# Performance work log

Hardware: AMD Instinct MI355X
Metric: run time of the kernel (lower is better)

## Reference

```python
import jax, jax.numpy as jnp
import numpy as np

LN_EPS = 1e-5

def _layer_norm(x, gamma, beta):
    mu = jnp.mean(x, axis=-1, keepdims=True)
    var = jnp.mean(jnp.square(x - mu), axis=-1, keepdims=True)
    return (x - mu) * jax.lax.rsqrt(var + LN_EPS) * gamma + beta

def setup_inputs() -> dict:
    key = jax.random.key(0)
    ks = jax.random.split(key, 6)
    B, Lc, S, H = 8, 16384, 2048, 256
    char_embeddings = jax.random.normal(ks[0], (B, Lc, H), dtype=jnp.float32)
    # include some negative indices (-1, -2) to exercise the no-token mask path
    token_alignment = jax.random.randint(ks[1], (B, Lc), -2, S, dtype=jnp.int32).astype(jnp.int64)
    decoder_hidden_states = jax.random.normal(ks[2], (B, S, H), dtype=jnp.float32)
    scale1 = 1.0 / np.sqrt(2 * H)
    W1 = jax.random.normal(ks[3], (2 * H, H), dtype=jnp.float32) * scale1
    b1 = jnp.zeros((H,), dtype=jnp.float32)
    W2 = jax.random.normal(ks[4], (2 * H, H), dtype=jnp.float32) * scale1
    b2 = jnp.zeros((H,), dtype=jnp.float32)
    ln_gamma = jnp.ones((H,), dtype=jnp.float32)
    ln_beta = jnp.zeros((H,), dtype=jnp.float32)
    return {
        "char_embeddings": char_embeddings,
        "token_alignment": token_alignment,
        "decoder_hidden_states": decoder_hidden_states,
        "W1": W1, "b1": b1, "W2": W2, "b2": b2,
        "ln_gamma": ln_gamma, "ln_beta": ln_beta,
    }

def reference(char_embeddings, token_alignment, decoder_hidden_states,
              W1, b1, W2, b2, ln_gamma, ln_beta):
    B, Lc, H = char_embeddings.shape
    S = decoder_hidden_states.shape[1]
    # per-character gather of decoder token representations (vectorized over batch)
    valid_idx = jnp.clip(token_alignment, 0, S - 1)                         # [B, Lc]
    tok_reprs = jnp.take_along_axis(decoder_hidden_states,
                                    valid_idx[..., None].astype(jnp.int32),
                                    axis=1)                                  # [B, Lc, H]
    tok_reprs = jnp.where((token_alignment < 0)[..., None], 0.0, tok_reprs)
    # alignment_network: Linear(2H -> H)
    combined = jnp.concatenate([char_embeddings, tok_reprs], axis=-1)        # [B, Lc, 2H]
    aligned = jnp.einsum('blk,kh->blh', combined, W1) + b1                   # [B, Lc, H]
    # syllable_feature_extractor: Linear(2H->H) + LayerNorm + GELU (+ eval-mode Dropout)
    combined2 = jnp.concatenate([char_embeddings, aligned], axis=-1)         # [B, Lc, 2H]
    feats = jnp.einsum('blk,kh->blh', combined2, W2) + b2
    feats = _layer_norm(feats, ln_gamma, ln_beta)
    feats = jax.nn.gelu(feats, approximate=False)                            # torch nn.GELU exact
    return char_embeddings + feats
```

## Files before the change

### kernel.cpp

```cpp
#include <hip/hip_runtime.h>
#include <hip/hip_bf16.h>
#include <math.h>
#include <stdint.h>

#define H     256
#define K2    512
#define SDEC  2048
#define LCSH  14
#define BM    64
#define BK    64
#define NTHR  256

typedef __attribute__((ext_vector_type(8))) short  short8;
typedef __attribute__((ext_vector_type(4))) float  f32x4;

typedef __attribute__((address_space(3))) unsigned int lds_u32;
typedef __attribute__((address_space(1))) unsigned int glb_u32;

__device__ __forceinline__ void async_ld16(const void* g, void* l) {
  __builtin_amdgcn_global_load_lds((const glb_u32*)(uintptr_t)g,
                                   (lds_u32*)(uintptr_t)l, 16, 0, 0);
}

__device__ __forceinline__ unsigned short f2bf(float f) {
  union { float f; unsigned int u; } c; c.f = f;
  unsigned int u = c.u;
  unsigned int r = u + 0x7fffu + ((u >> 16) & 1u);
  return (unsigned short)(r >> 16);
}

__global__ __launch_bounds__(256) void fuse_weights(
    const float* __restrict__ W1, const float* __restrict__ W2,
    unsigned short* __restrict__ wft) {
  __shared__ float As[64][65];
  __shared__ float Bs[64][65];
  const int t  = threadIdx.x;
  const int k0 = (blockIdx.x >> 2) * 64;
  const int n0 = (blockIdx.x & 3) * 64;
  const int lr = t >> 2;
  const int ls = t & 3;
  const int tk = t >> 4;
  const int tn = t & 15;

  float acc[4][4];
#pragma unroll
  for (int i = 0; i < 4; ++i)
#pragma unroll
    for (int c = 0; c < 4; ++c) acc[i][c] = 0.0f;

  for (int jt = 0; jt < 4; ++jt) {
    const int j0 = jt * 64;
    __syncthreads();
    const float* a_src = W1 + (size_t)(k0 + lr) * H + j0 + ls * 16;
    const float* b_src = W2 + (size_t)(H + j0 + lr) * H + n0 + ls * 16;
#pragma unroll
    for (int i = 0; i < 16; ++i) {
      As[lr][ls * 16 + i] = a_src[i];
      Bs[lr][ls * 16 + i] = b_src[i];
    }
    __syncthreads();
#pragma unroll 8
    for (int j = 0; j < 64; ++j) {
      float a[4], b[4];
#pragma unroll
      for (int i = 0; i < 4; ++i) a[i] = As[tk * 4 + i][j];
#pragma unroll
      for (int c = 0; c < 4; ++c) b[c] = Bs[j][tn * 4 + c];
#pragma unroll
      for (int i = 0; i < 4; ++i)
#pragma unroll
        for (int c = 0; c < 4; ++c) acc[i][c] += a[i] * b[c];
    }
  }

#pragma unroll
  for (int i = 0; i < 4; ++i) {
    const int k = k0 + tk * 4 + i;
#pragma unroll
    for (int c = 0; c < 4; ++c) {
      const int n = n0 + tn * 4 + c;
      float v = acc[i][c];
      if (k < H) v += W2[(size_t)k * H + n];
      wft[(size_t)n * K2 + k] = f2bf(v);
    }
  }
}

__global__ __launch_bounds__(256) void fuse_bias(
    const float* __restrict__ W2, const float* __restrict__ b1,
    const float* __restrict__ b2, float* __restrict__ biasf) {
  const int n = threadIdx.x;
  float acc = b2[n];
  for (int j = 0; j < H; ++j) acc += b1[j] * W2[(size_t)(H + j) * H + n];
  biasf[n] = acc;
}

__global__ __launch_bounds__(NTHR, 2) void syl_main(
    const float* __restrict__ cemb, const int* __restrict__ tal,
    const float* __restrict__ dec, const unsigned short* __restrict__ wft,
    const float* __restrict__ biasf, const float* __restrict__ gamma,
    const float* __restrict__ beta, float* __restrict__ out) {

  __shared__ __align__(16) unsigned short Ash[BM][72];
  __shared__ __align__(16) unsigned short Bsh[H][BK];
  __shared__ int   idxs[BM];
  __shared__ float msks[BM];
  __shared__ float stats[4][BM][2];

  const int t    = threadIdx.x;
  const int wave = t >> 6;
  const int lane = t & 63;
  const int quad = lane >> 4;
  const int l15  = lane & 15;
  const int row0 = blockIdx.x * BM;
  const int bidx = row0 >> LCSH;
  const float* decb = dec + (size_t)bidx * SDEC * H;

  if (t < BM) {
    int ix = tal[row0 + t];
    idxs[t] = ix < 0 ? 0 : (ix >= SDEC ? SDEC - 1 : ix);
    msks[t] = ix < 0 ? 0.0f : 1.0f;
  }

  f32x4 acc[4][4];
#pragma unroll
  for (int m = 0; m < 4; ++m)
#pragma unroll
    for (int n = 0; n < 4; ++n) acc[m][n] = (f32x4){0.f, 0.f, 0.f, 0.f};

  const int srow = t >> 2;
  const int sseg = t & 3;

  for (int ki = 0; ki < 8; ++ki) {
    const int k0 = ki * BK;

#pragma unroll
    for (int c = 0; c < 8; ++c) {
      const int nrow = wave * 64 + c * 8;
      const unsigned short* g =
          wft + (size_t)(nrow + (lane >> 3)) * K2 + k0 + (lane & 7) * 8;
      async_ld16(g, &Bsh[nrow][0]);
    }

    const float* src;
    float scale;
    if (k0 < H) {
      src = cemb + (size_t)(row0 + srow) * H + k0 + sseg * 16;
      scale = 1.0f;
    } else {
      src = decb + (size_t)idxs[srow] * H + (k0 - H) + sseg * 16;
      scale = msks[srow];
    }
    float4 f[4];
#pragma unroll
    for (int q = 0; q < 4; ++q) f[q] = *(const float4*)(src + q * 4);
    unsigned short hb[16];
#pragma unroll
    for (int q = 0; q < 4; ++q) {
      hb[q * 4 + 0] = f2bf(f[q].x * scale);
      hb[q * 4 + 1] = f2bf(f[q].y * scale);
      hb[q * 4 + 2] = f2bf(f[q].z * scale);
      hb[q * 4 + 3] = f2bf(f[q].w * scale);
    }
    *(short8*)&Ash[srow][sseg * 16]     = *(short8*)&hb[0];
    *(short8*)&Ash[srow][sseg * 16 + 8] = *(short8*)&hb[8];

    __syncthreads();

    short8 af[2][4];
#pragma unroll
    for (int ks = 0; ks < 2; ++ks)
#pragma unroll
      for (int m = 0; m < 4; ++m)
        af[ks][m] = *(const short8*)&Ash[m * 16 + l15][ks * 32 + quad * 8];
#pragma unroll
    for (int ks = 0; ks < 2; ++ks)
#pragma unroll
      for (int n = 0; n < 4; ++n) {
        short8 bf = *(const short8*)&Bsh[wave * 64 + n * 16 + l15][ks * 32 + quad * 8];
#pragma unroll
        for (int m = 0; m < 4; ++m)
          acc[m][n] = __builtin_amdgcn_mfma_f32_16x16x32_bf16(
              af[ks][m], bf, acc[m][n], 0, 0, 0);
      }
    __syncthreads();
  }

  float bvals[4], gvals[4], betv[4];
#pragma unroll
  for (int n = 0; n < 4; ++n) {
    const int col = wave * 64 + n * 16 + l15;
    bvals[n] = biasf[col];
    gvals[n] = gamma[col];
    betv[n]  = beta[col];
  }
#pragma unroll
  for (int m = 0; m < 4; ++m)
#pragma unroll
    for (int n = 0; n < 4; ++n)
#pragma unroll
      for (int r = 0; r < 4; ++r) acc[m][n][r] += bvals[n];

#pragma unroll
  for (int m = 0; m < 4; ++m)
#pragma unroll
    for (int r = 0; r < 4; ++r) {
      float a = 0.f, b = 0.f;
#pragma unroll
      for (int n = 0; n < 4; ++n) {
        const float v = acc[m][n][r];
        a += v; b += v * v;
      }
#pragma unroll
      for (int d = 1; d < 16; d <<= 1) {
        a += __shfl_xor(a, d, 64);
        b += __shfl_xor(b, d, 64);
      }
      if (l15 == 0) {
        const int row = m * 16 + quad * 4 + r;
        stats[wave][row][0] = a;
        stats[wave][row][1] = b;
      }
    }
  __syncthreads();

  float mean_[4][4], rstd_[4][4];
#pragma unroll
  for (int m = 0; m < 4; ++m)
#pragma unroll
    for (int r = 0; r < 4; ++r) {
      const int row = m * 16 + quad * 4 + r;
      const float a = stats[0][row][0] + stats[1][row][0] +
                      stats[2][row][0] + stats[3][row][0];
      const float b = stats[0][row][1] + stats[1][row][1] +
                      stats[2][row][1] + stats[3][row][1];
      const float mu  = a * (1.0f / 256.0f);
      const float var = b * (1.0f / 256.0f) - mu * mu;
      mean_[m][r] = mu;
      rstd_[m][r] = rsqrtf(var + 1e-5f);
    }

#pragma unroll
  for (int m = 0; m < 4; ++m) {
#pragma unroll
    for (int r = 0; r < 4; ++r) {
      const size_t row = (size_t)row0 + m * 16 + quad * 4 + r;
      const float* crow = cemb + row * H;
      float* orow = out + row * H;
#pragma unroll
      for (int n = 0; n < 4; ++n) {
        const int col = wave * 64 + n * 16 + l15;
        const float x = (acc[m][n][r] - mean_[m][r]) * rstd_[m][r];
        const float y = x * gvals[n] + betv[n];
        const float g = 0.5f * y * (1.0f + erff(y * 0.70710678118654752f));
        orow[col] = crow[col] + g;
      }
    }
  }
}

extern "C" void kernel_launch(void* const* d_in, const int* in_sizes, int n_in,
                              void* d_out, int out_size, void* d_ws, size_t ws_size,
                              hipStream_t stream) {
  const float* cemb  = (const float*)d_in[0];
  const int*   tal   = (const int*)d_in[1];
  const float* dec   = (const float*)d_in[2];
  const float* W1    = (const float*)d_in[3];
  const float* b1    = (const float*)d_in[4];
  const float* W2    = (const float*)d_in[5];
  const float* b2    = (const float*)d_in[6];
  const float* gamma = (const float*)d_in[7];
  const float* beta  = (const float*)d_in[8];
  float* out = (float*)d_out;

  unsigned short* wft = (unsigned short*)d_ws;
  float* biasf = (float*)((char*)d_ws + (size_t)K2 * H * sizeof(unsigned short));

  const int rows = in_sizes[0] / H;

  hipLaunchKernelGGL(fuse_weights, dim3(32), dim3(256), 0, stream, W1, W2, wft);
  hipLaunchKernelGGL(fuse_bias, dim3(1), dim3(256), 0, stream, W2, b1, b2, biasf);
  hipLaunchKernelGGL(syl_main, dim3(rows / BM), dim3(NTHR), 0, stream,
                     cemb, tal, dec, wft, biasf, gamma, beta, out);
}
```

Baseline: 405.8 us.

## Load B fragments from global into registers, double-buffer A, stage epilogue through LDS

The main GEMM kernel stops staging the fused weight tile in LDS. Each wave now reads its bf16 B fragments straight from global memory (L2-resident) into registers. The A tile is double-buffered in a fragment-ordered LDS layout, so the next K-slice's global loads overlap the current MFMAs, leaving one barrier per iteration. The epilogue writes GELU results into LDS and then emits coalesced float4 residual reads and output stores instead of scattered scalar accesses. Occupancy is raised to 3 blocks per SM through the smaller LDS footprint, at the cost of redundant per-wave weight loads from cache and extra barriers in the epilogue.

```diff
diff --git a/kernel.cpp b/kernel.cpp
--- a/kernel.cpp
+++ b/kernel.cpp
@@ -13,14 +13,6 @@
 
 typedef __attribute__((ext_vector_type(8))) short  short8;
 typedef __attribute__((ext_vector_type(4))) float  f32x4;
-
-typedef __attribute__((address_space(3))) unsigned int lds_u32;
-typedef __attribute__((address_space(1))) unsigned int glb_u32;
-
-__device__ __forceinline__ void async_ld16(const void* g, void* l) {
-  __builtin_amdgcn_global_load_lds((const glb_u32*)(uintptr_t)g,
-                                   (lds_u32*)(uintptr_t)l, 16, 0, 0);
-}
 
 __device__ __forceinline__ unsigned short f2bf(float f) {
   union { float f; unsigned int u; } c; c.f = f;
@@ -95,14 +87,16 @@
   biasf[n] = acc;
 }
 
-__global__ __launch_bounds__(NTHR, 2) void syl_main(
+__global__ __launch_bounds__(NTHR, 3) void syl_main(
     const float* __restrict__ cemb, const int* __restrict__ tal,
     const float* __restrict__ dec, const unsigned short* __restrict__ wft,
     const float* __restrict__ biasf, const float* __restrict__ gamma,
     const float* __restrict__ beta, float* __restrict__ out) {
 
-  __shared__ __align__(16) unsigned short Ash[BM][72];
-  __shared__ __align__(16) unsigned short Bsh[H][BK];
+  __shared__ __align__(16) char smem[16640];
+  unsigned short* AshC = (unsigned short*)smem;
+  float* Ef = (float*)smem;
+
   __shared__ int   idxs[BM];
   __shared__ float msks[BM];
   __shared__ float stats[4][BM][2];
@@ -130,60 +124,85 @@
 
   const int srow = t >> 2;
   const int sseg = t & 3;
-
+  const int ksS  = sseg >> 1;
+  const int qS   = (sseg & 1) * 2;
+  const int mS   = srow >> 4;
+  const int l15S = srow & 15;
+  const int wchunk0 = (ksS * 4 + mS) * 64 + qS * 16 + l15S;
+
+  {
+    const float* src = cemb + (size_t)(row0 + srow) * H + sseg * 16;
+    float4 f[4];
+#pragma unroll
+    for (int q = 0; q < 4; ++q) f[q] = *(const float4*)(src + q * 4);
+    unsigned short hb[16];
+#pragma unroll
+    for (int q = 0; q < 4; ++q) {
+      hb[q * 4 + 0] = f2bf(f[q].x); hb[q * 4 + 1] = f2bf(f[q].y);
+      hb[q * 4 + 2] = f2bf(f[q].z); hb[q * 4 + 3] = f2bf(f[q].w);
+    }
+    *(short8*)(AshC + (size_t)wchunk0 * 8)        = *(short8*)&hb[0];
+    *(short8*)(AshC + (size_t)(wchunk0 + 16) * 8) = *(short8*)&hb[8];
+  }
+  __syncthreads();
+
+  int buf = 0;
   for (int ki = 0; ki < 8; ++ki) {
     const int k0 = ki * BK;
 
-#pragma unroll
-    for (int c = 0; c < 8; ++c) {
-      const int nrow = wave * 64 + c * 8;
-      const unsigned short* g =
-          wft + (size_t)(nrow + (lane >> 3)) * K2 + k0 + (lane & 7) * 8;
-      async_ld16(g, &Bsh[nrow][0]);
-    }
-
-    const float* src;
-    float scale;
-    if (k0 < H) {
-      src = cemb + (size_t)(row0 + srow) * H + k0 + sseg * 16;
-      scale = 1.0f;
-    } else {
-      src = decb + (size_t)idxs[srow] * H + (k0 - H) + sseg * 16;
-      scale = msks[srow];
-    }
+    short8 bf[2][4];
+#pragma unroll
+    for (int ks = 0; ks < 2; ++ks)
+#pragma unroll
+      for (int n = 0; n < 4; ++n) {
+        const unsigned short* bp =
+            wft + (size_t)(wave * 64 + n * 16 + l15) * K2 + k0 + ks * 32 + quad * 8;
+        bf[ks][n] = *(const short8*)bp;
+      }
+
     float4 f[4];
-#pragma unroll
-    for (int q = 0; q < 4; ++q) f[q] = *(const float4*)(src + q * 4);
-    unsigned short hb[16];
-#pragma unroll
-    for (int q = 0; q < 4; ++q) {
-      hb[q * 4 + 0] = f2bf(f[q].x * scale);
-      hb[q * 4 + 1] = f2bf(f[q].y * scale);
-      hb[q * 4 + 2] = f2bf(f[q].z * scale);
-      hb[q * 4 + 3] = f2bf(f[q].w * scale);
-    }
-    *(short8*)&Ash[srow][sseg * 16]     = *(short8*)&hb[0];
-    *(short8*)&Ash[srow][sseg * 16 + 8] = *(short8*)&hb[8];
-
-    __syncthreads();
-
-    short8 af[2][4];
-#pragma unroll
-    for (int ks = 0; ks < 2; ++ks)
+    float scale = 1.0f;
+    if (ki < 7) {
+      const int k0n = k0 + BK;
+      const float* src;
+      if (k0n < H) {
+        src = cemb + (size_t)(row0 + srow) * H + k0n + sseg * 16;
+      } else {
+        src = decb + (size_t)idxs[srow] * H + (k0n - H) + sseg * 16;
+        scale = msks[srow];
+      }
+#pragma unroll
+      for (int q = 0; q < 4; ++q) f[q] = *(const float4*)(src + q * 4);
+    }
+
+#pragma unroll
+    for (int ks = 0; ks < 2; ++ks) {
+      short8 af[4];
 #pragma unroll
       for (int m = 0; m < 4; ++m)
-        af[ks][m] = *(const short8*)&Ash[m * 16 + l15][ks * 32 + quad * 8];
-#pragma unroll
-    for (int ks = 0; ks < 2; ++ks)
-#pragma unroll
-      for (int n = 0; n < 4; ++n) {
-        short8 bf = *(const short8*)&Bsh[wave * 64 + n * 16 + l15][ks * 32 + quad * 8];
+        af[m] = *(const short8*)(AshC +
+                 (size_t)(((buf * 2 + ks) * 4 + m) * 64 + lane) * 8);
+#pragma unroll
+      for (int n = 0; n < 4; ++n)
 #pragma unroll
         for (int m = 0; m < 4; ++m)
           acc[m][n] = __builtin_amdgcn_mfma_f32_16x16x32_bf16(
-              af[ks][m], bf, acc[m][n], 0, 0, 0);
-      }
-    __syncthreads();
+              af[m], bf[ks][n], acc[m][n], 0, 0, 0);
+    }
+
+    if (ki < 7) {
+      unsigned short hb[16];
+#pragma unroll
+      for (int q = 0; q < 4; ++q) {
+        hb[q * 4 + 0] = f2bf(f[q].x * scale); hb[q * 4 + 1] = f2bf(f[q].y * scale);
+        hb[q * 4 + 2] = f2bf(f[q].z * scale); hb[q * 4 + 3] = f2bf(f[q].w * scale);
+      }
+      const int nb = buf ^ 1;
+      *(short8*)(AshC + (size_t)(nb * 512 + wchunk0) * 8)      = *(short8*)&hb[0];
+      *(short8*)(AshC + (size_t)(nb * 512 + wchunk0 + 16) * 8) = *(short8*)&hb[8];
+      __syncthreads();
+      buf = nb;
+    }
   }
 
   float bvals[4], gvals[4], betv[4];
@@ -240,22 +259,34 @@
       rstd_[m][r] = rsqrtf(var + 1e-5f);
     }
 
+  const int erow = t >> 4;
+  const int eseg = t & 15;
 #pragma unroll
   for (int m = 0; m < 4; ++m) {
 #pragma unroll
     for (int r = 0; r < 4; ++r) {
-      const size_t row = (size_t)row0 + m * 16 + quad * 4 + r;
-      const float* crow = cemb + row * H;
-      float* orow = out + row * H;
 #pragma unroll
       for (int n = 0; n < 4; ++n) {
-        const int col = wave * 64 + n * 16 + l15;
         const float x = (acc[m][n][r] - mean_[m][r]) * rstd_[m][r];
         const float y = x * gvals[n] + betv[n];
         const float g = 0.5f * y * (1.0f + erff(y * 0.70710678118654752f));
-        orow[col] = crow[col] + g;
-      }
-    }
+        Ef[(quad * 4 + r) * 260 + wave * 64 + n * 16 + l15] = g;
+      }
+    }
+    __syncthreads();
+    {
+      const size_t grow = (size_t)row0 + m * 16 + erow;
+      const float* crow = cemb + grow * H + eseg * 16;
+      float* orow = out + grow * H + eseg * 16;
+#pragma unroll
+      for (int j = 0; j < 4; ++j) {
+        float4 v = *(const float4*)&Ef[erow * 260 + eseg * 16 + j * 4];
+        float4 c = *(const float4*)(crow + j * 4);
+        v.x += c.x; v.y += c.y; v.z += c.z; v.w += c.w;
+        *(float4*)(orow + j * 4) = v;
+      }
+    }
+    __syncthreads();
   }
 }
 
```

New measurement: 401.7 us. No clear change (-1.0%).

## Pre-convert inputs to bf16 and load MFMA operands directly from global memory

Applied to the files above, without the earlier changes.

Adds a conversion kernel that writes bf16 copies of char embeddings and decoder states into workspace. The main kernel drops LDS staging and barriers and loads A and B MFMA fragments straight from global memory. It also reads the residual from the bf16 copy instead of fp32. The aim is less memory traffic and no synchronisation in the K loop. The cost is an extra full pass over the inputs, more uncoalesced per-lane global loads, and a precision loss in the residual add. A fallback keeps on-the-fly conversion when the workspace is too small.

```diff
diff --git a/kernel.cpp b/kernel.cpp
--- a/kernel.cpp
+++ b/kernel.cpp
@@ -1,32 +1,24 @@
 #include <hip/hip_runtime.h>
-#include <hip/hip_bf16.h>
 #include <math.h>
 #include <stdint.h>
 
 #define H     256
 #define K2    512
 #define SDEC  2048
-#define LCSH  14
-#define BM    64
-#define BK    64
 #define NTHR  256
 
 typedef __attribute__((ext_vector_type(8))) short  short8;
 typedef __attribute__((ext_vector_type(4))) float  f32x4;
-
-typedef __attribute__((address_space(3))) unsigned int lds_u32;
-typedef __attribute__((address_space(1))) unsigned int glb_u32;
-
-__device__ __forceinline__ void async_ld16(const void* g, void* l) {
-  __builtin_amdgcn_global_load_lds((const glb_u32*)(uintptr_t)g,
-                                   (lds_u32*)(uintptr_t)l, 16, 0, 0);
-}
 
 __device__ __forceinline__ unsigned short f2bf(float f) {
   union { float f; unsigned int u; } c; c.f = f;
   unsigned int u = c.u;
   unsigned int r = u + 0x7fffu + ((u >> 16) & 1u);
   return (unsigned short)(r >> 16);
+}
+__device__ __forceinline__ float bf2f(unsigned short h) {
+  union { unsigned int u; float f; } c; c.u = ((unsigned int)h) << 16;
+  return c.f;
 }
 
 __global__ __launch_bounds__(256) void fuse_weights(
@@ -95,31 +87,44 @@
   biasf[n] = acc;
 }
 
-__global__ __launch_bounds__(NTHR, 2) void syl_main(
+__global__ __launch_bounds__(256) void conv_bf16(
+    const float* __restrict__ src, unsigned short* __restrict__ dst, int n4) {
+  const int i = blockIdx.x * 256 + threadIdx.x;
+  if (i < n4) {
+    const float4 f = ((const float4*)src)[i];
+    uint2 o;
+    o.x = (unsigned int)f2bf(f.x) | ((unsigned int)f2bf(f.y) << 16);
+    o.y = (unsigned int)f2bf(f.z) | ((unsigned int)f2bf(f.w) << 16);
+    ((uint2*)dst)[i] = o;
+  }
+}
+
+template <bool PRE>
+__global__ __launch_bounds__(NTHR, 3) void syl_main(
     const float* __restrict__ cemb, const int* __restrict__ tal,
-    const float* __restrict__ dec, const unsigned short* __restrict__ wft,
-    const float* __restrict__ biasf, const float* __restrict__ gamma,
-    const float* __restrict__ beta, float* __restrict__ out) {
-
-  __shared__ __align__(16) unsigned short Ash[BM][72];
-  __shared__ __align__(16) unsigned short Bsh[H][BK];
-  __shared__ int   idxs[BM];
-  __shared__ float msks[BM];
-  __shared__ float stats[4][BM][2];
+    const float* __restrict__ dec, const unsigned short* __restrict__ cembh,
+    const unsigned short* __restrict__ dech,
+    const unsigned short* __restrict__ wft, const float* __restrict__ biasf,
+    const float* __restrict__ gamma, const float* __restrict__ beta,
+    float* __restrict__ out) {
+
+  __shared__ float stats[4][64][2];
 
   const int t    = threadIdx.x;
   const int wave = t >> 6;
   const int lane = t & 63;
   const int quad = lane >> 4;
   const int l15  = lane & 15;
-  const int row0 = blockIdx.x * BM;
-  const int bidx = row0 >> LCSH;
-  const float* decb = dec + (size_t)bidx * SDEC * H;
-
-  if (t < BM) {
-    int ix = tal[row0 + t];
-    idxs[t] = ix < 0 ? 0 : (ix >= SDEC ? SDEC - 1 : ix);
-    msks[t] = ix < 0 ? 0.0f : 1.0f;
+  const int row0 = blockIdx.x * 64;
+  const int bidx = blockIdx.x >> 8;
+
+  int  tok[4];
+  bool msk[4];
+#pragma unroll
+  for (int m = 0; m < 4; ++m) {
+    const int ix = tal[row0 + m * 16 + l15];
+    msk[m] = ix >= 0;
+    tok[m] = ix < 0 ? 0 : (ix >= SDEC ? SDEC - 1 : ix);
   }
 
   f32x4 acc[4][4];
@@ -128,62 +133,66 @@
 #pragma unroll
     for (int n = 0; n < 4; ++n) acc[m][n] = (f32x4){0.f, 0.f, 0.f, 0.f};
 
-  const int srow = t >> 2;
-  const int sseg = t & 3;
-
+  const short8 z8 = (short8)0;
+
+#pragma unroll
   for (int ki = 0; ki < 8; ++ki) {
-    const int k0 = ki * BK;
-
-#pragma unroll
-    for (int c = 0; c < 8; ++c) {
-      const int nrow = wave * 64 + c * 8;
-      const unsigned short* g =
-          wft + (size_t)(nrow + (lane >> 3)) * K2 + k0 + (lane & 7) * 8;
-      async_ld16(g, &Bsh[nrow][0]);
-    }
-
-    const float* src;
-    float scale;
-    if (k0 < H) {
-      src = cemb + (size_t)(row0 + srow) * H + k0 + sseg * 16;
-      scale = 1.0f;
-    } else {
-      src = decb + (size_t)idxs[srow] * H + (k0 - H) + sseg * 16;
-      scale = msks[srow];
-    }
-    float4 f[4];
-#pragma unroll
-    for (int q = 0; q < 4; ++q) f[q] = *(const float4*)(src + q * 4);
-    unsigned short hb[16];
-#pragma unroll
-    for (int q = 0; q < 4; ++q) {
-      hb[q * 4 + 0] = f2bf(f[q].x * scale);
-      hb[q * 4 + 1] = f2bf(f[q].y * scale);
-      hb[q * 4 + 2] = f2bf(f[q].z * scale);
-      hb[q * 4 + 3] = f2bf(f[q].w * scale);
-    }
-    *(short8*)&Ash[srow][sseg * 16]     = *(short8*)&hb[0];
-    *(short8*)&Ash[srow][sseg * 16 + 8] = *(short8*)&hb[8];
-
-    __syncthreads();
-
-    short8 af[2][4];
-#pragma unroll
-    for (int ks = 0; ks < 2; ++ks)
-#pragma unroll
-      for (int m = 0; m < 4; ++m)
-        af[ks][m] = *(const short8*)&Ash[m * 16 + l15][ks * 32 + quad * 8];
-#pragma unroll
-    for (int ks = 0; ks < 2; ++ks)
-#pragma unroll
-      for (int n = 0; n < 4; ++n) {
-        short8 bf = *(const short8*)&Bsh[wave * 64 + n * 16 + l15][ks * 32 + quad * 8];
+#pragma unroll
+    for (int ks = 0; ks < 2; ++ks) {
+      const int kk = ki * 64 + ks * 32;
+      short8 af[4], bf[4];
+
+      if (kk < H) {
+#pragma unroll
+        for (int m = 0; m < 4; ++m) {
+          if (PRE) {
+            af[m] = *(const short8*)(cembh +
+                     (size_t)(row0 + m * 16 + l15) * H + kk + quad * 8);
+          } else {
+            const float* p = cemb + (size_t)(row0 + m * 16 + l15) * H + kk + quad * 8;
+            const float4 lo = *(const float4*)p;
+            const float4 hi = *(const float4*)(p + 4);
+            short8 a;
+            a[0] = (short)f2bf(lo.x); a[1] = (short)f2bf(lo.y);
+            a[2] = (short)f2bf(lo.z); a[3] = (short)f2bf(lo.w);
+            a[4] = (short)f2bf(hi.x); a[5] = (short)f2bf(hi.y);
+            a[6] = (short)f2bf(hi.z); a[7] = (short)f2bf(hi.w);
+            af[m] = a;
+          }
+        }
+      } else {
+#pragma unroll
+        for (int m = 0; m < 4; ++m) {
+          if (PRE) {
+            short8 a = *(const short8*)(dech +
+                        (size_t)(bidx * SDEC + tok[m]) * H + (kk - H) + quad * 8);
+            af[m] = msk[m] ? a : z8;
+          } else {
+            const float* p = dec + (size_t)(bidx * SDEC + tok[m]) * H + (kk - H) + quad * 8;
+            const float4 lo = *(const float4*)p;
+            const float4 hi = *(const float4*)(p + 4);
+            short8 a;
+            a[0] = (short)f2bf(lo.x); a[1] = (short)f2bf(lo.y);
+            a[2] = (short)f2bf(lo.z); a[3] = (short)f2bf(lo.w);
+            a[4] = (short)f2bf(hi.x); a[5] = (short)f2bf(hi.y);
+            a[6] = (short)f2bf(hi.z); a[7] = (short)f2bf(hi.w);
+            af[m] = msk[m] ? a : z8;
+          }
+        }
+      }
+
+#pragma unroll
+      for (int n = 0; n < 4; ++n)
+        bf[n] = *(const short8*)(wft +
+                 (size_t)(wave * 64 + n * 16 + l15) * K2 + kk + quad * 8);
+
+#pragma unroll
+      for (int n = 0; n < 4; ++n)
 #pragma unroll
         for (int m = 0; m < 4; ++m)
           acc[m][n] = __builtin_amdgcn_mfma_f32_16x16x32_bf16(
-              af[ks][m], bf, acc[m][n], 0, 0, 0);
-      }
-    __syncthreads();
+              af[m], bf[n], acc[m][n], 0, 0, 0);
+    }
   }
 
   float bvals[4], gvals[4], betv[4];
@@ -224,36 +233,31 @@
     }
   __syncthreads();
 
-  float mean_[4][4], rstd_[4][4];
-#pragma unroll
-  for (int m = 0; m < 4; ++m)
+#pragma unroll
+  for (int m = 0; m < 4; ++m) {
 #pragma unroll
     for (int r = 0; r < 4; ++r) {
-      const int row = m * 16 + quad * 4 + r;
-      const float a = stats[0][row][0] + stats[1][row][0] +
-                      stats[2][row][0] + stats[3][row][0];
-      const float b = stats[0][row][1] + stats[1][row][1] +
-                      stats[2][row][1] + stats[3][row][1];
-      const float mu  = a * (1.0f / 256.0f);
-      const float var = b * (1.0f / 256.0f) - mu * mu;
-      mean_[m][r] = mu;
-      rstd_[m][r] = rsqrtf(var + 1e-5f);
-    }
-
-#pragma unroll
-  for (int m = 0; m < 4; ++m) {
-#pragma unroll
-    for (int r = 0; r < 4; ++r) {
-      const size_t row = (size_t)row0 + m * 16 + quad * 4 + r;
-      const float* crow = cemb + row * H;
-      float* orow = out + row * H;
+      const int rloc = m * 16 + quad * 4 + r;
+      const float a = stats[0][rloc][0] + stats[1][rloc][0] +
+                      stats[2][rloc][0] + stats[3][rloc][0];
+      const float b = stats[0][rloc][1] + stats[1][rloc][1] +
+                      stats[2][rloc][1] + stats[3][rloc][1];
+      const float mu   = a * (1.0f / 256.0f);
+      const float var  = b * (1.0f / 256.0f) - mu * mu;
+      const float rstd = rsqrtf(var + 1e-5f);
+
+      const size_t grow = (size_t)row0 + rloc;
+      const float* crow = cemb + grow * H;
+      const unsigned short* chrow = cembh + grow * H;
+      float* orow = out + grow * H;
 #pragma unroll
       for (int n = 0; n < 4; ++n) {
         const int col = wave * 64 + n * 16 + l15;
-        const float x = (acc[m][n][r] - mean_[m][r]) * rstd_[m][r];
+        const float x = (acc[m][n][r] - mu) * rstd;
         const float y = x * gvals[n] + betv[n];
         const float g = 0.5f * y * (1.0f + erff(y * 0.70710678118654752f));
-        orow[col] = crow[col] + g;
+        const float res = PRE ? bf2f(chrow[col]) : crow[col];
+        orow[col] = res + g;
       }
     }
   }
@@ -273,13 +277,29 @@
   const float* beta  = (const float*)d_in[8];
   float* out = (float*)d_out;
 
-  unsigned short* wft = (unsigned short*)d_ws;
-  float* biasf = (float*)((char*)d_ws + (size_t)K2 * H * sizeof(unsigned short));
-
-  const int rows = in_sizes[0] / H;
+  const int rows  = in_sizes[0] / H;
+  const int ncemb = in_sizes[0];
+  const int ndec  = in_sizes[2];
+
+  unsigned short* wft  = (unsigned short*)d_ws;
+  float* biasf = (float*)((char*)d_ws + 262144);
+  unsigned short* cembh = (unsigned short*)((char*)d_ws + 263168);
+  unsigned short* dech  = (unsigned short*)((char*)d_ws + 263168 + (size_t)ncemb * 2);
+  const size_t need = 263168 + (size_t)ncemb * 2 + (size_t)ndec * 2;
 
   hipLaunchKernelGGL(fuse_weights, dim3(32), dim3(256), 0, stream, W1, W2, wft);
   hipLaunchKernelGGL(fuse_bias, dim3(1), dim3(256), 0, stream, W2, b1, b2, biasf);
-  hipLaunchKernelGGL(syl_main, dim3(rows / BM), dim3(NTHR), 0, stream,
-                     cemb, tal, dec, wft, biasf, gamma, beta, out);
-}
+
+  if (ws_size >= need) {
+    hipLaunchKernelGGL(conv_bf16, dim3((ncemb / 4 + 255) / 256), dim3(256), 0,
+                       stream, cemb, cembh, ncemb / 4);
+    hipLaunchKernelGGL(conv_bf16, dim3((ndec / 4 + 255) / 256), dim3(256), 0,
+                       stream, dec, dech, ndec / 4);
+    hipLaunchKernelGGL((syl_main<true>), dim3(rows / 64), dim3(NTHR), 0, stream,
+                       cemb, tal, dec, cembh, dech, wft, biasf, gamma, beta, out);
+  } else {
+    hipLaunchKernelGGL((syl_main<false>), dim3(rows / 64), dim3(NTHR), 0, stream,
+                       cemb, tal, dec, (const unsigned short*)nullptr,
+                       (const unsigned short*)nullptr, wft, biasf, gamma, beta, out);
+  }
+}
```

Result: slower. 438.9 us (+8.2%).
